# Kernel optimization log

Hardware: AMD Instinct MI355X
Metric: run time of the kernel (lower is better)

Reference implementation:

```python
import jax, jax.numpy as jnp
import numpy as np

EMBED = 1024
HEADS = 16
HEAD_DIM = EMBED // HEADS


def setup_inputs() -> dict:
    key = jax.random.key(0)
    ks = jax.random.split(key, 11)
    B, S = 4, 2048
    scale = 1.0 / np.sqrt(EMBED)
    inp = {
        "query": jax.random.normal(ks[0], (B, S, EMBED), dtype=jnp.float32),
        "key": jax.random.normal(ks[1], (B, S, EMBED), dtype=jnp.float32),
        "value": jax.random.normal(ks[2], (B, S, EMBED), dtype=jnp.float32),
        "Wq": jax.random.normal(ks[3], (EMBED, EMBED), dtype=jnp.float32) * scale,
        "bq": jnp.zeros((EMBED,), dtype=jnp.float32),
        "Wk": jax.random.normal(ks[4], (EMBED, EMBED), dtype=jnp.float32) * scale,
        "bk": jnp.zeros((EMBED,), dtype=jnp.float32),
        "Wv": jax.random.normal(ks[5], (EMBED, EMBED), dtype=jnp.float32) * scale,
        "bv": jnp.zeros((EMBED,), dtype=jnp.float32),
        "Wo": jax.random.normal(ks[6], (EMBED, EMBED), dtype=jnp.float32) * scale,
        "bo": jnp.zeros((EMBED,), dtype=jnp.float32),
    }
    return inp


def _split_heads(x):
    # [B,S,E] -> [B,H,S,D]
    B, S, _ = x.shape
    return x.reshape(B, S, HEADS, HEAD_DIM).transpose(0, 2, 1, 3)


def reference(query, key, value, Wq, bq, Wk, bk, Wv, bv, Wo, bo):
    B, S, _ = query.shape
    q = _split_heads(query @ Wq.T + bq)   # [B,H,S,D]
    k = _split_heads(key @ Wk.T + bk)
    v = _split_heads(value @ Wv.T + bv)
    scores = jnp.einsum("bhqd,bhkd->bhqk", q, k) / jnp.sqrt(jnp.float32(HEAD_DIM))
    attn = jax.nn.softmax(scores, axis=-1)
    out = jnp.einsum("bhqk,bhkd->bhqd", attn, v)  # [B,H,S,D]
    out = out.transpose(0, 2, 1, 3).reshape(B, S, EMBED)
    return out @ Wo.T + bo
```

## Files before the change

### kernel.cpp

```cpp
#include <hip/hip_runtime.h>

typedef _Float16 f16;
typedef __attribute__((ext_vector_type(2))) __fp16 fp16x2_raw;
typedef __attribute__((ext_vector_type(4))) _Float16 f16x4;
typedef __attribute__((ext_vector_type(8))) _Float16 f16x8;
typedef __attribute__((ext_vector_type(4))) float f32x4;
typedef __attribute__((ext_vector_type(16))) float f32x16;
typedef __attribute__((ext_vector_type(2))) unsigned int u32x2;

#define NB 4
#define NS 2048
#define NE 1024
#define NH 16
#define ND 64
#define NM (NB*NS)

__device__ __forceinline__ void gld16(const void* g, void* l) {
  __builtin_amdgcn_global_load_lds((const __attribute__((address_space(1))) unsigned int*)g,
                                   (__attribute__((address_space(3))) unsigned int*)l, 16, 0, 0);
}

__device__ __forceinline__ unsigned cvt2h(float a, float b) {
  fp16x2_raw r = __builtin_amdgcn_cvt_pkrtz(a, b);
  return __builtin_bit_cast(unsigned, r);
}

__device__ __forceinline__ void plswap(unsigned& a, unsigned& b) {
  asm volatile("v_permlane32_swap_b32 %0, %1" : "+v"(a), "+v"(b));
}

__global__ __launch_bounds__(256) void cvt_all(const float* __restrict__ s0, const float* __restrict__ s1,
                                               const float* __restrict__ s2, const float* __restrict__ s3,
                                               const float* __restrict__ s4, const float* __restrict__ s5,
                                               const float* __restrict__ s6, f16* __restrict__ dst) {
  const int X = NM*NE/4;
  const int W = NE*NE/4;
  const int total = 3*X + 4*W;
  int idx = blockIdx.x * blockDim.x + threadIdx.x;
  int stride = gridDim.x * blockDim.x;
  for (int i = idx; i < total; i += stride) {
    const float* src; int off;
    if      (i <   X)     { src = s0; off = i; }
    else if (i < 2*X)     { src = s1; off = i - X; }
    else if (i < 3*X)     { src = s2; off = i - 2*X; }
    else if (i < 3*X+W)   { src = s3; off = i - 3*X; }
    else if (i < 3*X+2*W) { src = s4; off = i - (3*X+W); }
    else if (i < 3*X+3*W) { src = s5; off = i - (3*X+2*W); }
    else                  { src = s6; off = i - (3*X+3*W); }
    float4 v = ((const float4*)src)[off];
    f16x4 o;
    o[0] = (_Float16)v.x; o[1] = (_Float16)v.y; o[2] = (_Float16)v.z; o[3] = (_Float16)v.w;
    ((f16x4*)dst)[i] = o;
  }
}

template<bool OUTF32>
__global__ __launch_bounds__(256)
void gemm_bt(const f16* __restrict__ A, const f16* __restrict__ Bw,
             const float* __restrict__ bias, float* __restrict__ Cf,
             f16* __restrict__ Ch, int M, int N, int K)
{
  __shared__ __align__(16) f16 As[128*32];
  __shared__ __align__(16) f16 Bs[128*32];
  const int t = threadIdx.x;
  const int l = t & 63, w = t >> 6;
  const int wr = w >> 1, wc = w & 1;

  const int id = blockIdx.x + blockIdx.y * gridDim.x;
  const int xcd = id & 7, slot = id >> 3;
  const int m0 = (((slot >> 3) << 3) | xcd) * 128;
  const int n0 = (slot & 7) * 128;

  f32x4 acc[4][4];
  #pragma unroll
  for (int i = 0; i < 4; ++i)
    #pragma unroll
    for (int j = 0; j < 4; ++j)
      acc[i][j] = f32x4{0.f, 0.f, 0.f, 0.f};

  const int off0 = (w*2+0)*1024 + l*16;
  const int off1 = (w*2+1)*1024 + l*16;
  const int row0 = off0 >> 6, k0 = (off0 & 63) >> 1;
  const int row1 = off1 >> 6, k1 = (off1 & 63) >> 1;
  const f16* a0 = A  + (size_t)(m0+row0)*K + k0;
  const f16* a1 = A  + (size_t)(m0+row1)*K + k1;
  const f16* b0 = Bw + (size_t)(n0+row0)*K + k0;
  const f16* b1 = Bw + (size_t)(n0+row1)*K + k1;
  f16* As0 = As + off0/2; f16* As1 = As + off1/2;
  f16* Bs0 = Bs + off0/2; f16* Bs1 = Bs + off1/2;

  const int aoff = (wr*64 + (l&15))*32 + ((l>>4)<<3);
  const int boff = (wc*64 + (l&15))*32 + ((l>>4)<<3);

  for (int kt = 0; kt < K; kt += 32) {
    __syncthreads();
    gld16(a0 + kt, As0);
    gld16(a1 + kt, As1);
    gld16(b0 + kt, Bs0);
    gld16(b1 + kt, Bs1);
    __syncthreads();
    f16x8 af[4], bf[4];
    #pragma unroll
    for (int i = 0; i < 4; ++i) af[i] = *(const f16x8*)(As + aoff + i*512);
    #pragma unroll
    for (int j = 0; j < 4; ++j) bf[j] = *(const f16x8*)(Bs + boff + j*512);
    #pragma unroll
    for (int i = 0; i < 4; ++i)
      #pragma unroll
      for (int j = 0; j < 4; ++j)
        acc[i][j] = __builtin_amdgcn_mfma_f32_16x16x32_f16(af[i], bf[j], acc[i][j], 0, 0, 0);
  }

  #pragma unroll
  for (int j = 0; j < 4; ++j) {
    const int col = n0 + wc*64 + j*16 + (l & 15);
    const float bb = bias[col];
    #pragma unroll
    for (int i = 0; i < 4; ++i) {
      const int rowb = m0 + wr*64 + i*16 + ((l>>4)<<2);
      #pragma unroll
      for (int r = 0; r < 4; ++r) {
        float v = acc[i][j][r] + bb;
        if constexpr (OUTF32) Cf[(size_t)(rowb+r)*N + col] = v;
        else                  Ch[(size_t)(rowb+r)*N + col] = (f16)v;
      }
    }
  }
}

__global__ __launch_bounds__(256, 4)
void attn_kernel(const f16* __restrict__ Q, const f16* __restrict__ K,
                 const f16* __restrict__ V, f16* __restrict__ O)
{
  __shared__ __align__(16) f16 S_lds[16384];

  const int t = threadIdx.x, l = t & 63, w = t >> 6;
  const int lq = l & 31, hi = l >> 5;

  const int lin = blockIdx.x + (blockIdx.y << 4);
  const int xcd = lin & 7, jj = lin >> 3;
  const int bh = xcd * 8 + (jj >> 4);
  const int qt = jj & 15;
  const int b = bh >> 4, h = bh & 15;
  const size_t base = (size_t)b * NS * NE + (size_t)h * ND;
  const int q = qt*128 + w*32 + lq;

  f16x8 bq[4];
  #pragma unroll
  for (int ks = 0; ks < 4; ++ks)
    bq[ks] = *(const f16x8*)&Q[base + (size_t)q*NE + ks*16 + hi*8];
  asm volatile("s_waitcnt vmcnt(0)" ::: "memory");

  f32x16 o[2];
  #pragma unroll
  for (int dt = 0; dt < 2; ++dt)
    #pragma unroll
    for (int r = 0; r < 16; ++r) o[dt][r] = 0.f;
  float m2 = -3e38f, lsum = 0.f;
  const float K2 = 0.125f * 1.44269504089f;

  const int krow0 = w*16 + (l>>3);
  const int kgran = ((l&7) ^ (l>>3)) * 8;
  const f16* kSrc0 = K + base + (size_t)krow0*NE + kgran;
  const f16* kSrc1 = kSrc0 + (size_t)8*NE;
  const f16* vSrc = V + base + (size_t)l*NE + w*16;

  const size_t tileAdv = (size_t)64 * NE;
  const int kd0 = (w*2+0)*512 + l*8;
  const int kd1 = (w*2+1)*512 + l*8;

  f16x8 va, vb;
  {
    gld16(kSrc0, &S_lds[0] + kd0);
    gld16(kSrc1, &S_lds[0] + kd1);
    va = *(const f16x8*)(vSrc);
    vb = *(const f16x8*)(vSrc + 8);
    asm volatile("s_waitcnt vmcnt(0)" ::: "memory");
    char* vt0 = (char*)&S_lds[4096];
    #pragma unroll
    for (int i = 0; i < 8; ++i) {
      const int d0 = w*16 + i, d1 = w*16 + 8 + i;
      *(f16*)(vt0 + ((d0*128 + l*2) ^ ((i & 7) << 4))) = va[i];
      *(f16*)(vt0 + ((d1*128 + l*2) ^ ((i & 7) << 4))) = vb[i];
    }
  }
  __syncthreads();

  for (int it = 0; it < 32; ++it) {
    const int cur = it & 1, nb = cur ^ 1;
    const char* ksb = (const char*)(&S_lds[cur*8192]);
    const char* vtb = (const char*)(&S_lds[cur*8192 + 4096]);

    if (it < 31) {
      const size_t g = (size_t)(it+1) * tileAdv;
      gld16(kSrc0 + g, &S_lds[nb*8192] + kd0);
      gld16(kSrc1 + g, &S_lds[nb*8192] + kd1);
      va = *(const f16x8*)(vSrc + g);
      vb = *(const f16x8*)(vSrc + g + 8);
    }

    f32x16 s[2];
    #pragma unroll
    for (int ct = 0; ct < 2; ++ct)
      #pragma unroll
      for (int r = 0; r < 16; ++r) s[ct][r] = 0.f;
    __builtin_amdgcn_s_setprio(1);
    #pragma unroll
    for (int ct = 0; ct < 2; ++ct) {
      const int krow = ct*32 + lq;
      const int rswz = (krow & 7) << 4;
      #pragma unroll
      for (int ks = 0; ks < 4; ++ks) {
        f16x8 ak = *(const f16x8*)(ksb + ((krow*128 + ks*32 + hi*16) ^ rswz));
        s[ct] = __builtin_amdgcn_mfma_f32_32x32x16_f16(ak, bq[ks], s[ct], 0, 0, 0);
      }
    }
    __builtin_amdgcn_s_setprio(0);

    float mm[16];
    #pragma unroll
    for (int r = 0; r < 16; ++r) mm[r] = fmaxf(s[0][r], s[1][r]);
    #pragma unroll
    for (int st = 8; st > 0; st >>= 1)
      #pragma unroll
      for (int r = 0; r < st; ++r) mm[r] = fmaxf(mm[r], mm[r+st]);
    float mx = mm[0] * K2;
    mx = fmaxf(mx, __shfl_xor(mx, 32));

    if (__any(mx > m2 + 8.0f)) {
      const float mnew = fmaxf(m2, mx);
      const float alpha = __builtin_amdgcn_exp2f(m2 - mnew);
      m2 = mnew;
      lsum *= alpha;
      #pragma unroll
      for (int dt = 0; dt < 2; ++dt)
        #pragma unroll
        for (int r = 0; r < 16; ++r) o[dt][r] *= alpha;
    }

    float ps4[4] = {0.f, 0.f, 0.f, 0.f};
    #pragma unroll
    for (int ct = 0; ct < 2; ++ct)
      #pragma unroll
      for (int r = 0; r < 16; ++r) {
        float p = __builtin_amdgcn_exp2f(s[ct][r]*K2 - m2);
        s[ct][r] = p;
        ps4[r & 3] += p;
      }
    lsum += (ps4[0] + ps4[1]) + (ps4[2] + ps4[3]);

    f16x8 pa[4];
    #pragma unroll
    for (int ct = 0; ct < 2; ++ct) {
      unsigned wd[8];
      #pragma unroll
      for (int m = 0; m < 4; ++m)
        #pragma unroll
        for (int hh = 0; hh < 2; ++hh)
          wd[m*2 + hh] = cvt2h(s[ct][4*m + 2*hh], s[ct][4*m + 2*hh + 1]);
      #pragma unroll
      for (int ks2 = 0; ks2 < 2; ++ks2) {
        unsigned a0 = wd[(2*ks2)*2 + 0], b0 = wd[(2*ks2+1)*2 + 0];
        unsigned a1 = wd[(2*ks2)*2 + 1], b1 = wd[(2*ks2+1)*2 + 1];
        plswap(a0, b0);
        plswap(a1, b1);
        union { unsigned u[4]; f16x8 v; } pp;
        pp.u[0] = a0; pp.u[1] = a1; pp.u[2] = b0; pp.u[3] = b1;
        pa[ct*2 + ks2] = pp.v;
      }
    }

    __builtin_amdgcn_s_setprio(1);
    #pragma unroll
    for (int ks = 0; ks < 4; ++ks)
      #pragma unroll
      for (int dt = 0; dt < 2; ++dt) {
        const int drow = dt*32 + lq;
        f16x8 av = *(const f16x8*)(vtb + ((drow*128 + ks*32 + hi*16) ^ ((drow & 7) << 4)));
        o[dt] = __builtin_amdgcn_mfma_f32_32x32x16_f16(av, pa[ks], o[dt], 0, 0, 0);
      }
    __builtin_amdgcn_s_setprio(0);

    if (it < 31) {
      asm volatile("s_waitcnt vmcnt(0)" ::: "memory");
      char* vtn = (char*)(&S_lds[nb*8192 + 4096]);
      #pragma unroll
      for (int i = 0; i < 8; ++i) {
        const int d0 = w*16 + i, d1 = w*16 + 8 + i;
        *(f16*)(vtn + ((d0*128 + l*2) ^ ((i & 7) << 4))) = va[i];
        *(f16*)(vtn + ((d1*128 + l*2) ^ ((i & 7) << 4))) = vb[i];
      }
      __syncthreads();
    }
  }

  const float lt = lsum + __shfl_xor(lsum, 32);
  const float linv = 1.0f / lt;
  #pragma unroll
  for (int dt = 0; dt < 2; ++dt)
    #pragma unroll
    for (int m = 0; m < 4; ++m) {
      u32x2 st;
      st.x = cvt2h(o[dt][4*m+0]*linv, o[dt][4*m+1]*linv);
      st.y = cvt2h(o[dt][4*m+2]*linv, o[dt][4*m+3]*linv);
      const int d = dt*32 + 8*m + 4*hi;
      *(u32x2*)&O[base + (size_t)q*NE + d] = st;
    }
}

extern "C" void kernel_launch(void* const* d_in, const int* in_sizes, int n_in,
                              void* d_out, int out_size, void* d_ws, size_t ws_size,
                              hipStream_t stream)
{
  const float* q_in = (const float*)d_in[0];
  const float* k_in = (const float*)d_in[1];
  const float* v_in = (const float*)d_in[2];
  const float* Wq = (const float*)d_in[3];
  const float* bq = (const float*)d_in[4];
  const float* Wk = (const float*)d_in[5];
  const float* bk = (const float*)d_in[6];
  const float* Wv = (const float*)d_in[7];
  const float* bv = (const float*)d_in[8];
  const float* Wo = (const float*)d_in[9];
  const float* bo = (const float*)d_in[10];

  char* ws = (char*)d_ws;
  f16* Xq   = (f16*)(ws + 0);
  f16* Xk   = (f16*)(ws + 16777216);
  f16* Xv   = (f16*)(ws + 33554432);
  f16* Wq16 = (f16*)(ws + 50331648);
  f16* Wk16 = (f16*)(ws + 52428800);
  f16* Wv16 = (f16*)(ws + 54525952);
  f16* Wo16 = (f16*)(ws + 56623104);
  f16* Qp   = (f16*)(ws + 58720256);
  f16* Kp   = (f16*)(ws + 75497472);
  f16* Vp   = (f16*)(ws + 92274688);
  f16* Op   = (f16*)(ws + 109051904);

  cvt_all<<<2048, 256, 0, stream>>>(q_in, k_in, v_in, Wq, Wk, Wv, Wo, Xq);

  dim3 gg(8, 64);
  gemm_bt<false><<<gg, 256, 0, stream>>>(Xq, Wq16, bq, nullptr, Qp, NM, NE, NE);
  gemm_bt<false><<<gg, 256, 0, stream>>>(Xk, Wk16, bk, nullptr, Kp, NM, NE, NE);
  gemm_bt<false><<<gg, 256, 0, stream>>>(Xv, Wv16, bv, nullptr, Vp, NM, NE, NE);

  attn_kernel<<<dim3(16, 64), 256, 0, stream>>>(Qp, Kp, Vp, Op);

  gemm_bt<true><<<gg, 256, 0, stream>>>(Op, Wo16, bo, (float*)d_out, nullptr, NM, NE, NE);
}
```

Before: 252.9 us.

## Split attention KV range across two wave groups with LDS merge

Doubles the attention block to 512 threads. Two groups of four waves each process half of the key/value sequence for the same 128 queries, and the partial softmax states are merged through LDS at the end. Each group now uses its own single LDS buffer instead of the previous double buffer, so global loads are no longer prefetched and each iteration syncs twice. The intent is more parallelism and occupancy per query tile, paid for with lost load/compute overlap and an extra merge step.

```diff
diff --git a/kernel.cpp b/kernel.cpp
--- a/kernel.cpp
+++ b/kernel.cpp
@@ -128,13 +128,18 @@
   }
 }
 
-__global__ __launch_bounds__(256, 4)
+__global__ __launch_bounds__(512, 8)
 void attn_kernel(const f16* __restrict__ Q, const f16* __restrict__ K,
                  const f16* __restrict__ V, f16* __restrict__ O)
 {
   __shared__ __align__(16) f16 S_lds[16384];
-
-  const int t = threadIdx.x, l = t & 63, w = t >> 6;
+  __shared__ float m_lds[4][32];
+  __shared__ float l_lds[4][32];
+
+  const int t = threadIdx.x, l = t & 63;
+  const int w6 = t >> 6;
+  const int grp = w6 >> 2;
+  const int wg = w6 & 3;
   const int lq = l & 31, hi = l >> 5;
 
   const int lin = blockIdx.x + (blockIdx.y << 4);
@@ -143,7 +148,8 @@
   const int qt = jj & 15;
   const int b = bh >> 4, h = bh & 15;
   const size_t base = (size_t)b * NS * NE + (size_t)h * ND;
-  const int q = qt*128 + w*32 + lq;
+  const int q = qt*128 + wg*32 + lq;
+  const int koff = grp * (NS/2);
 
   f16x8 bq[4];
   #pragma unroll
@@ -159,45 +165,36 @@
   float m2 = -3e38f, lsum = 0.f;
   const float K2 = 0.125f * 1.44269504089f;
 
-  const int krow0 = w*16 + (l>>3);
+  const int krow0 = wg*16 + (l>>3);
   const int kgran = ((l&7) ^ (l>>3)) * 8;
-  const f16* kSrc0 = K + base + (size_t)krow0*NE + kgran;
+  const f16* kSrc0 = K + base + (size_t)(koff + krow0)*NE + kgran;
   const f16* kSrc1 = kSrc0 + (size_t)8*NE;
-  const f16* vSrc = V + base + (size_t)l*NE + w*16;
+  const f16* vSrc = V + base + (size_t)(koff + l)*NE + wg*16;
+
+  f16* gK = &S_lds[grp*8192];
+  f16* kDst0 = gK + (wg*2+0)*512 + l*8;
+  f16* kDst1 = gK + (wg*2+1)*512 + l*8;
+  const char* ksb = (const char*)gK;
+  char* vtb = (char*)(gK + 4096);
 
   const size_t tileAdv = (size_t)64 * NE;
-  const int kd0 = (w*2+0)*512 + l*8;
-  const int kd1 = (w*2+1)*512 + l*8;
-
-  f16x8 va, vb;
-  {
-    gld16(kSrc0, &S_lds[0] + kd0);
-    gld16(kSrc1, &S_lds[0] + kd1);
-    va = *(const f16x8*)(vSrc);
-    vb = *(const f16x8*)(vSrc + 8);
-    asm volatile("s_waitcnt vmcnt(0)" ::: "memory");
-    char* vt0 = (char*)&S_lds[4096];
-    #pragma unroll
-    for (int i = 0; i < 8; ++i) {
-      const int d0 = w*16 + i, d1 = w*16 + 8 + i;
-      *(f16*)(vt0 + ((d0*128 + l*2) ^ ((i & 7) << 4))) = va[i];
-      *(f16*)(vt0 + ((d1*128 + l*2) ^ ((i & 7) << 4))) = vb[i];
-    }
-  }
-  __syncthreads();
-
-  for (int it = 0; it < 32; ++it) {
-    const int cur = it & 1, nb = cur ^ 1;
-    const char* ksb = (const char*)(&S_lds[cur*8192]);
-    const char* vtb = (const char*)(&S_lds[cur*8192 + 4096]);
-
-    if (it < 31) {
-      const size_t g = (size_t)(it+1) * tileAdv;
-      gld16(kSrc0 + g, &S_lds[nb*8192] + kd0);
-      gld16(kSrc1 + g, &S_lds[nb*8192] + kd1);
-      va = *(const f16x8*)(vSrc + g);
-      vb = *(const f16x8*)(vSrc + g + 8);
-    }
+
+  for (int it = 0; it < 16; ++it) {
+    const size_t g = (size_t)it * tileAdv;
+    __syncthreads();
+    gld16(kSrc0 + g, kDst0);
+    gld16(kSrc1 + g, kDst1);
+    {
+      f16x8 va = *(const f16x8*)(vSrc + g);
+      f16x8 vb = *(const f16x8*)(vSrc + g + 8);
+      #pragma unroll
+      for (int i = 0; i < 8; ++i) {
+        const int d0 = wg*16 + i, d1 = wg*16 + 8 + i;
+        *(f16*)(vtb + ((d0*128 + l*2) ^ ((i & 7) << 4))) = va[i];
+        *(f16*)(vtb + ((d1*128 + l*2) ^ ((i & 7) << 4))) = vb[i];
+      }
+    }
+    __syncthreads();
 
     f32x16 s[2];
     #pragma unroll
@@ -280,32 +277,49 @@
         o[dt] = __builtin_amdgcn_mfma_f32_32x32x16_f16(av, pa[ks], o[dt], 0, 0, 0);
       }
     __builtin_amdgcn_s_setprio(0);
-
-    if (it < 31) {
-      asm volatile("s_waitcnt vmcnt(0)" ::: "memory");
-      char* vtn = (char*)(&S_lds[nb*8192 + 4096]);
-      #pragma unroll
-      for (int i = 0; i < 8; ++i) {
-        const int d0 = w*16 + i, d1 = w*16 + 8 + i;
-        *(f16*)(vtn + ((d0*128 + l*2) ^ ((i & 7) << 4))) = va[i];
-        *(f16*)(vtn + ((d1*128 + l*2) ^ ((i & 7) << 4))) = vb[i];
-      }
-      __syncthreads();
-    }
   }
 
   const float lt = lsum + __shfl_xor(lsum, 32);
-  const float linv = 1.0f / lt;
-  #pragma unroll
-  for (int dt = 0; dt < 2; ++dt)
-    #pragma unroll
-    for (int m = 0; m < 4; ++m) {
-      u32x2 st;
-      st.x = cvt2h(o[dt][4*m+0]*linv, o[dt][4*m+1]*linv);
-      st.y = cvt2h(o[dt][4*m+2]*linv, o[dt][4*m+3]*linv);
-      const int d = dt*32 + 8*m + 4*hi;
-      *(u32x2*)&O[base + (size_t)q*NE + d] = st;
-    }
+
+  __syncthreads();
+
+  if (grp == 1) {
+    float* ow = (float*)&S_lds[0];
+    #pragma unroll
+    for (int dt = 0; dt < 2; ++dt)
+      #pragma unroll
+      for (int k = 0; k < 16; ++k) {
+        const int j = dt*16 + k;
+        ow[wg*2048 + l*32 + (j ^ (l & 31))] = o[dt][k];
+      }
+    if (hi == 0) { m_lds[wg][lq] = m2; l_lds[wg][lq] = lt; }
+  }
+  __syncthreads();
+
+  if (grp == 0) {
+    const float* orp = (const float*)&S_lds[0];
+    const float m_b = m_lds[wg][lq];
+    const float l_b = l_lds[wg][lq];
+    const float ms = fmaxf(m2, m_b);
+    const float sa = __builtin_amdgcn_exp2f(m2 - ms);
+    const float sb = __builtin_amdgcn_exp2f(m_b - ms);
+    const float lstar = lt*sa + l_b*sb;
+    const float linv = 1.0f / lstar;
+    #pragma unroll
+    for (int dt = 0; dt < 2; ++dt)
+      #pragma unroll
+      for (int m = 0; m < 4; ++m) {
+        float v0 = (o[dt][4*m+0]*sa + orp[wg*2048 + l*32 + ((dt*16+4*m+0) ^ (l&31))]*sb) * linv;
+        float v1 = (o[dt][4*m+1]*sa + orp[wg*2048 + l*32 + ((dt*16+4*m+1) ^ (l&31))]*sb) * linv;
+        float v2 = (o[dt][4*m+2]*sa + orp[wg*2048 + l*32 + ((dt*16+4*m+2) ^ (l&31))]*sb) * linv;
+        float v3 = (o[dt][4*m+3]*sa + orp[wg*2048 + l*32 + ((dt*16+4*m+3) ^ (l&31))]*sb) * linv;
+        u32x2 st;
+        st.x = cvt2h(v0, v1);
+        st.y = cvt2h(v2, v3);
+        const int d = dt*32 + 8*m + 4*hi;
+        *(u32x2*)&O[base + (size_t)q*NE + d] = st;
+      }
+  }
 }
 
 extern "C" void kernel_launch(void* const* d_in, const int* in_sizes, int n_in,
@@ -344,7 +358,7 @@
   gemm_bt<false><<<gg, 256, 0, stream>>>(Xk, Wk16, bk, nullptr, Kp, NM, NE, NE);
   gemm_bt<false><<<gg, 256, 0, stream>>>(Xv, Wv16, bv, nullptr, Vp, NM, NE, NE);
 
-  attn_kernel<<<dim3(16, 64), 256, 0, stream>>>(Qp, Kp, Vp, Op);
+  attn_kernel<<<dim3(16, 64), 512, 0, stream>>>(Qp, Kp, Vp, Op);
 
   gemm_bt<true><<<gg, 256, 0, stream>>>(Op, Wo16, bo, (float*)d_out, nullptr, NM, NE, NE);
 }
```

After: 724.1 us. +186.3%, slower.
